# Optimization experiments

Hardware: AMD Instinct MI355X
Metric: run time of the kernel (lower is better)

The kernel has to match this reference:

```python
import jax, jax.numpy as jnp
import numpy as np

B, N, D = 4, 4096, 64   # batch, num points, point-feature channels
K = 24                  # original_k_neighbors
GO = 128                # graph_out_channel = max(32, (D*2//8)*8)
MLP = [64, 128, 256]
HALF = MLP[-1] // 2     # graph_feature_mapping out channels
EPS = 1e-5

def leaky(x):
    return jnp.where(x > 0, x, 0.2 * x)

def bn(x, gamma, beta, axes):
    # training-mode batch norm (biased variance, like torch normalization); channel last
    m = jnp.mean(x, axes, keepdims=True)
    v = jnp.var(x, axes, keepdims=True)
    return (x - m) * jax.lax.rsqrt(v + EPS) * gamma + beta

def knn_idx(p, k):
    # p: [B,N,3] -> indices of k nearest neighbors (self excluded), [B,N,k]
    sq = jnp.sum(p * p, -1)
    dist = sq[:, :, None] + sq[:, None, :] - 2.0 * jnp.einsum('bnc,bmc->bnm', p, p)
    _, idx = jax.lax.top_k(-dist, k + 1)   # smallest k+1 distances
    return idx[:, :, 1:]

def setup_inputs():
    key = jax.random.key(0)
    ks = jax.random.split(key, 8)
    w = lambda i, s: jax.random.normal(ks[i], s, jnp.float32) * 0.05
    return {
        'xyz': jax.random.normal(ks[0], (B, 3, N), jnp.float32),
        'points': jax.random.normal(ks[1], (B, D, N), jnp.float32),
        'ec_w': w(2, (GO, 2 * D)),
        'ec_g': jnp.ones((GO,), jnp.float32), 'ec_b': jnp.zeros((GO,), jnp.float32),
        'gm_w': w(3, (HALF, GO)),
        'gm_g': jnp.ones((HALF,), jnp.float32), 'gm_b': jnp.zeros((HALF,), jnp.float32),
        'w0': w(4, (MLP[0], D + 3)), 'bias0': jnp.zeros((MLP[0],), jnp.float32),
        'g0': jnp.ones((MLP[0],), jnp.float32), 'be0': jnp.zeros((MLP[0],), jnp.float32),
        'w1': w(5, (MLP[1], MLP[0])), 'bias1': jnp.zeros((MLP[1],), jnp.float32),
        'g1': jnp.ones((MLP[1],), jnp.float32), 'be1': jnp.zeros((MLP[1],), jnp.float32),
        'w2': w(6, (MLP[2], MLP[1])), 'bias2': jnp.zeros((MLP[2],), jnp.float32),
        'g2': jnp.ones((MLP[2],), jnp.float32), 'be2': jnp.zeros((MLP[2],), jnp.float32),
        'fu_w': w(7, (MLP[2], MLP[2] + HALF)),
        'fu_g': jnp.ones((MLP[2],), jnp.float32), 'fu_b': jnp.zeros((MLP[2],), jnp.float32),
    }

def reference(xyz, points, ec_w, ec_g, ec_b, gm_w, gm_g, gm_b,
              w0, bias0, g0, be0, w1, bias1, g1, be1, w2, bias2, g2, be2,
              fu_w, fu_g, fu_b):
    xyz_t = jnp.transpose(xyz, (0, 2, 1))     # [B,N,3]
    pts_t = jnp.transpose(points, (0, 2, 1))  # [B,N,D]
    edges = knn_idx(xyz_t, K)                 # [B,N,K]
    # --- EdgeConv on original graph ---
    nb = jax.vmap(lambda f, e: f[e])(pts_t, edges)  # gather: [B,N,K,D]
    ctr = pts_t[:, :, None, :]
    ef = jnp.concatenate([jnp.broadcast_to(ctr, nb.shape), nb - ctr], -1)  # [B,N,K,2D]
    h = jnp.einsum('bnkc,oc->bnko', ef, ec_w)
    h = leaky(bn(h, ec_g, ec_b, (0, 1, 2)))
    gfeat = jnp.max(h, axis=2)                # max over neighbors -> [B,N,GO]
    # --- graph_feature_mapping ---
    gm = jnp.einsum('bnc,oc->bno', gfeat, gm_w)
    gm = leaky(bn(gm, gm_g, gm_b, (0, 1)))    # [B,N,HALF]
    # --- group_all PointNet MLP ---
    g = jnp.concatenate([xyz_t, pts_t], -1)   # [B,N,D+3]
    for wl, bl, gl, bel in ((w0, bias0, g0, be0), (w1, bias1, g1, be1), (w2, bias2, g2, be2)):
        g = jax.nn.relu(bn(jnp.einsum('bnc,oc->bno', g, wl) + bl, gl, bel, (0, 1)))
    point_feat = jnp.max(g, axis=1)           # [B, MLP[-1]]
    graph_glob = jnp.max(gm, axis=1)          # [B, HALF]
    # --- fusion ---
    fused = jnp.concatenate([point_feat, graph_glob], -1)
    f = jnp.einsum('bc,oc->bo', fused, fu_w)
    f = leaky(bn(f, fu_g, fu_b, (0,)))
    return f[:, :, None]                      # [B, MLP[-1], 1]
```

## Files before the change

### kernel.cpp

```cpp
#include <hip/hip_runtime.h>

#define NPTS 4096
#define QN   16384
#define KNN  24

static constexpr size_t OFF_EDGES = 0;
static constexpr size_t OFF_BIG   = 393216;
static constexpr size_t OFF_A     = OFF_BIG;
static constexpr size_t OFF_C     = OFF_BIG + 2097152;
static constexpr size_t OFF_M     = OFF_BIG + 4194304;
static constexpr size_t OFF_GM    = OFF_BIG + 6553600;
static constexpr size_t OFF_L0    = OFF_GM + 2097152;
static constexpr size_t OFF_L1    = OFF_L0 + 1048576;
static constexpr size_t OFF_L2    = OFF_L1 + 2097152;
static constexpr size_t ST_BASE   = OFF_L2 + 4194304;
static constexpr size_t ST_BN1    = ST_BASE;
static constexpr size_t ST_GM     = ST_BASE + 256;
static constexpr size_t ST_L0     = ST_BASE + 512;
static constexpr size_t ST_L1     = ST_BASE + 640;
static constexpr size_t ST_L2     = ST_BASE + 896;
static constexpr size_t OFF_PF    = ST_BASE + 1408;
static constexpr size_t OFF_GG    = ST_BASE + 2432;
static constexpr size_t ST_TICKET = ST_BASE + 2944;
static constexpr int    ST_COUNT  = 2945;

__device__ inline unsigned fmap(float f) {
    unsigned u = __float_as_uint(f);
    return (u & 0x80000000u) ? ~u : (u | 0x80000000u);
}
__device__ inline float funmap(unsigned u) {
    unsigned v = (u & 0x80000000u) ? (u & 0x7fffffffu) : ~u;
    return __uint_as_float(v);
}

__device__ inline void xcd_decode(int v, int& b, int& t) {
    b = (v & 7) >> 1;
    t = ((v >> 3) << 1) | (v & 1);
}

template<int I, int O, int OH, int MODE, bool HASBIAS>
__device__ void layer_part(unsigned char* smem, int b, int chunk, int o0,
    const float* __restrict__ inraw, const float* __restrict__ inst, float rcnt,
    const float* __restrict__ ing, const float* __restrict__ inbe,
    const float* __restrict__ W, const float* __restrict__ bias,
    const float* __restrict__ xyz, const float* __restrict__ pts,
    float* __restrict__ outraw, float* __restrict__ outst)
{
    constexpr int OW = OH / 16;
    constexpr int OP = OH + 4;
    float* ns  = (float*)smem;
    float* nb  = ns + I;
    float* inl = nb + I;
    float* wl  = inl + 64 * 65;
    int q0 = b * 4096 + chunk * 64;

    if (MODE != 0) {
        if (threadIdx.x < I) {
            int c = threadIdx.x;
            float m = inst[c] * rcnt;
            float v = inst[I + c] * rcnt - m * m;
            float inv = 1.0f / sqrtf(v + 1e-5f);
            float sc = inv * ing[c];
            ns[c] = sc;
            nb[c] = inbe[c] - m * sc;
        }
    }

    int ng = threadIdx.x & 15, og = threadIdx.x >> 4;
    float acc[4][OW];
    #pragma unroll
    for (int r = 0; r < 4; ++r)
        #pragma unroll
        for (int i = 0; i < OW; ++i) acc[r][i] = 0.f;

    for (int ct = 0; ct < I; ct += 64) {
        int CT = (I - ct < 64) ? (I - ct) : 64;
        __syncthreads();
        if (MODE == 0) {
            for (int idx = threadIdx.x; idx < CT * 64; idx += 256) {
                int c = idx >> 6, p = idx & 63;
                int ch = ct + c;
                float v = (ch < 3) ? xyz[((size_t)(b * 3 + ch) << 12) + chunk * 64 + p]
                                   : pts[((size_t)(b * 64 + ch - 3) << 12) + chunk * 64 + p];
                inl[p * 65 + c] = v;
            }
        } else {
            const float* src = inraw + (size_t)q0 * I + ct;
            for (int idx = threadIdx.x; idx < 64 * 64; idx += 256) {
                int p = idx >> 6, c = idx & 63;
                if (c < CT) {
                    float v = fmaf(src[(size_t)p * I + c], ns[ct + c], nb[ct + c]);
                    v = (MODE == 1) ? fmaxf(v, 0.0f) : ((v > 0.0f) ? v : 0.2f * v);
                    inl[p * 65 + c] = v;
                }
            }
        }
        if (CT == 64) {
            for (int idx = threadIdx.x; idx < 64 * OH; idx += 256) {
                int o = idx >> 6, cc = idx & 63;
                wl[cc * OP + o] = W[(size_t)(o0 + o) * I + ct + cc];
            }
        } else {
            for (int idx = threadIdx.x; idx < CT * OH; idx += 256) {
                int o = idx / CT, cc = idx - o * CT;
                wl[cc * OP + o] = W[(size_t)(o0 + o) * I + ct + cc];
            }
        }
        __syncthreads();
        for (int cc = 0; cc < CT; ++cc) {
            float pv[4];
            #pragma unroll
            for (int r = 0; r < 4; ++r) pv[r] = inl[(ng * 4 + r) * 65 + cc];
            const float* wr = &wl[cc * OP + og * OW];
            if constexpr (OW == 4) {
                float4 wv = *(const float4*)wr;
                #pragma unroll
                for (int r = 0; r < 4; ++r) {
                    acc[r][0] = fmaf(pv[r], wv.x, acc[r][0]);
                    acc[r][1] = fmaf(pv[r], wv.y, acc[r][1]);
                    acc[r][2] = fmaf(pv[r], wv.z, acc[r][2]);
                    acc[r][3] = fmaf(pv[r], wv.w, acc[r][3]);
                }
            } else {
                float2 wv = *(const float2*)wr;
                #pragma unroll
                for (int r = 0; r < 4; ++r) {
                    acc[r][0] = fmaf(pv[r], wv.x, acc[r][0]);
                    acc[r][1] = fmaf(pv[r], wv.y, acc[r][1]);
                }
            }
        }
    }

    if (HASBIAS) {
        #pragma unroll
        for (int i = 0; i < OW; ++i) {
            float bv = bias[o0 + og * OW + i];
            #pragma unroll
            for (int r = 0; r < 4; ++r) acc[r][i] += bv;
        }
    }
    __syncthreads();
    #pragma unroll
    for (int r = 0; r < 4; ++r)
        #pragma unroll
        for (int i = 0; i < OW; ++i)
            wl[(ng * 4 + r) * OP + og * OW + i] = acc[r][i];
    __syncthreads();

    for (int idx = threadIdx.x; idx < 64 * OH; idx += 256) {
        int p = idx / OH, o = idx - p * OH;
        outraw[(size_t)(q0 + p) * O + o0 + o] = wl[p * OP + o];
    }
    if (threadIdx.x < OH) {
        int o = threadIdx.x;
        float s1 = 0.f, s2 = 0.f;
        #pragma unroll 8
        for (int p = 0; p < 64; ++p) {
            float v = wl[p * OP + o];
            s1 += v;
            s2 = fmaf(v, v, s2);
        }
        atomicAdd(&outst[o0 + o], s1);
        atomicAdd(&outst[O + o0 + o], s2);
    }
}

__global__ __launch_bounds__(256) void kA(const float* __restrict__ xyz,
                                          const float* __restrict__ pts,
                                          const float* __restrict__ ec_w,
                                          int* __restrict__ edges,
                                          float* __restrict__ afeat,
                                          float* __restrict__ cfeat,
                                          float* __restrict__ stz) {
    __shared__ __align__(16) unsigned char smem[25856];
    int u = blockIdx.x;
    if (u < 4096) {
        float4* cand = (float4*)smem;
        unsigned long long* bufall = (unsigned long long*)(smem + 16384);
        int b = u >> 10;
        int wave = threadIdx.x >> 6, lane = threadIdx.x & 63;
        int n = ((u & 1023) << 2) + wave;
        const float* xb = xyz + (size_t)b * 3 * 4096;
        unsigned long long* wbuf = bufall + wave * 128;

        float xq = xb[n], yq = xb[4096 + n], zq = xb[8192 + n];
        float sqq = __fadd_rn(__fadd_rn(__fmul_rn(xq, xq), __fmul_rn(yq, yq)), __fmul_rn(zq, zq));

        unsigned T = 0xFFFFFFFFu;
        int count = 0;

        auto reduce = [&]() {
            unsigned long long ka = (lane < count) ? wbuf[lane] : ~0ull;
            int ra = 0;
            if (count > 64) {
                unsigned long long kb = (lane + 64 < count) ? wbuf[lane + 64] : ~0ull;
                int rb = 0;
                for (int j = 0; j < count; ++j) {
                    unsigned long long kj = wbuf[j];
                    ra += (kj < ka);
                    rb += (kj < kb);
                }
                if (rb < 25) wbuf[rb] = kb;
            } else {
                for (int j = 0; j < count; ++j) {
                    unsigned long long kj = wbuf[j];
                    ra += (kj < ka);
                }
            }
            if (ra < 25) wbuf[ra] = ka;
            count = 25;
            T = (unsigned)(wbuf[24] >> 32);
        };

        for (int strip = 0; strip < 4; ++strip) {
            __syncthreads();
            for (int i = threadIdx.x; i < 1024; i += 256) {
                int j = strip * 1024 + i;
                float x = xb[j], y = xb[4096 + j], z = xb[8192 + j];
                float sq = __fadd_rn(__fadd_rn(__fmul_rn(x, x), __fmul_rn(y, y)), __fmul_rn(z, z));
                cand[i] = make_float4(x, y, z, sq);
            }
            __syncthreads();
            for (int t = 0; t < 16; ++t) {
                float4 cv = cand[t * 64 + lane];
                float dot = __fadd_rn(__fadd_rn(__fmul_rn(xq, cv.x), __fmul_rn(yq, cv.y)), __fmul_rn(zq, cv.z));
                float d = __fsub_rn(__fadd_rn(sqq, cv.w), __fmul_rn(2.0f, dot));
                unsigned du = fmap(d);
                bool surv = (du <= T);
                unsigned long long m = __ballot(surv);
                if (m) {
                    if (surv) {
                        int ofs = __popcll(m & ((1ull << lane) - 1ull));
                        unsigned idx = (unsigned)(strip * 1024 + t * 64 + lane);
                        wbuf[count + ofs] = ((unsigned long long)du << 32) | idx;
                    }
                    count += (int)__popcll(m);
                    if (count >= 64) reduce();
                }
            }
        }
        reduce();
        if (lane >= 1 && lane < 25)
            edges[((size_t)(b * 4096 + n)) * KNN + lane - 1] = (int)(unsigned)(wbuf[lane] & 0xFFFFFFFFull);
    } else if (u < 6144) {
        int v = u - 4096;
        int b, t;
        xcd_decode(v, b, t);
        int nchunk = t & 63, sub = t >> 6;
        int which = sub >> 2;
        int o0 = (sub & 3) * 32;
        int n0 = nchunk * 64;

        float* inl = (float*)smem;
        float* wl  = (float*)(smem + 16640);
        const float* pb = pts + (size_t)b * 64 * 4096;

        for (int idx = threadIdx.x; idx < 64 * 64; idx += 256) {
            int c = idx >> 6, p = idx & 63;
            inl[p * 65 + c] = pb[(size_t)c * 4096 + n0 + p];
        }
        for (int idx = threadIdx.x; idx < 64 * 32; idx += 256) {
            int cc = idx & 63, o = idx >> 6;
            float w2v = ec_w[(o0 + o) * 128 + 64 + cc];
            wl[cc * 36 + o] = which ? w2v : (ec_w[(o0 + o) * 128 + cc] - w2v);
        }
        __syncthreads();

        int ng = threadIdx.x & 15, og = threadIdx.x >> 4;
        float acc[4][2] = {{0.f, 0.f}, {0.f, 0.f}, {0.f, 0.f}, {0.f, 0.f}};
        for (int cc = 0; cc < 64; ++cc) {
            float pv[4];
            #pragma unroll
            for (int r = 0; r < 4; ++r) pv[r] = inl[(ng * 4 + r) * 65 + cc];
            float2 wv = *(const float2*)&wl[cc * 36 + og * 2];
            #pragma unroll
            for (int r = 0; r < 4; ++r) {
                acc[r][0] = fmaf(pv[r], wv.x, acc[r][0]);
                acc[r][1] = fmaf(pv[r], wv.y, acc[r][1]);
            }
        }
        __syncthreads();
        #pragma unroll
        for (int r = 0; r < 4; ++r) {
            wl[(ng * 4 + r) * 36 + og * 2 + 0] = acc[r][0];
            wl[(ng * 4 + r) * 36 + og * 2 + 1] = acc[r][1];
        }
        __syncthreads();
        float* dst = (which ? cfeat : afeat) + ((size_t)(b * 4096 + n0)) * 128 + o0;
        for (int idx = threadIdx.x; idx < 64 * 32; idx += 256) {
            int p = idx >> 5, o = idx & 31;
            dst[(size_t)p * 128 + o] = wl[p * 36 + o];
        }
    } else {
        for (int i = threadIdx.x; i < ST_COUNT; i += 256) stz[i] = 0.f;
    }
}

__global__ __launch_bounds__(256) void kB(const float* __restrict__ afeat,
                                          const float* __restrict__ cfeat,
                                          const int* __restrict__ edges,
                                          float* __restrict__ M,
                                          float* __restrict__ stBN1,
                                          const float* __restrict__ xyz,
                                          const float* __restrict__ pts,
                                          const float* __restrict__ w0,
                                          const float* __restrict__ bias0,
                                          float* __restrict__ l0raw,
                                          float* __restrict__ stL0) {
    __shared__ __align__(16) unsigned char smem[26368];
    int u = blockIdx.x;
    if (u < 1024) {
        int* eL = (int*)smem;
        float* red = (float*)(smem + 1536);
        int b, chunk;
        xcd_decode(u, b, chunk);
        int q0 = b * 4096 + chunk * 16;
        for (int idx = threadIdx.x; idx < 16 * KNN; idx += 256) eL[idx] = edges[(size_t)q0 * KNN + idx];
        __syncthreads();

        int m = threadIdx.x & 31;
        int g = threadIdx.x >> 5;
        int bbase = b << 12;
        float s1[4] = {0.f, 0.f, 0.f, 0.f}, s2[4] = {0.f, 0.f, 0.f, 0.f};

        #pragma unroll
        for (int half = 0; half < 2; ++half) {
            int p = g + half * 8;
            int q = q0 + p;
            float mx0 = -__builtin_inff(), mx1 = mx0, mx2 = mx0, mx3 = mx0;
            float sv0 = 0.f, sv1 = 0.f, sv2 = 0.f, sv3 = 0.f;
            float qv0 = 0.f, qv1 = 0.f, qv2 = 0.f, qv3 = 0.f;
            #pragma unroll 8
            for (int k = 0; k < KNN; ++k) {
                int e = eL[p * KNN + k];
                float4 v = *(const float4*)&cfeat[((size_t)(bbase + e) << 7) + m * 4];
                mx0 = fmaxf(mx0, v.x); sv0 += v.x; qv0 = fmaf(v.x, v.x, qv0);
                mx1 = fmaxf(mx1, v.y); sv1 += v.y; qv1 = fmaf(v.y, v.y, qv1);
                mx2 = fmaxf(mx2, v.z); sv2 += v.z; qv2 = fmaf(v.z, v.z, qv2);
                mx3 = fmaxf(mx3, v.w); sv3 += v.w; qv3 = fmaf(v.w, v.w, qv3);
            }
            float4 a = *(const float4*)&afeat[((size_t)q << 7) + m * 4];
            float4 mo = make_float4(a.x + mx0, a.y + mx1, a.z + mx2, a.w + mx3);
            *(float4*)&M[((size_t)q << 7) + m * 4] = mo;
            s1[0] += fmaf(24.f, a.x, sv0); s2[0] += 24.f * a.x * a.x + 2.f * a.x * sv0 + qv0;
            s1[1] += fmaf(24.f, a.y, sv1); s2[1] += 24.f * a.y * a.y + 2.f * a.y * sv1 + qv1;
            s1[2] += fmaf(24.f, a.z, sv2); s2[2] += 24.f * a.z * a.z + 2.f * a.z * sv2 + qv2;
            s1[3] += fmaf(24.f, a.w, sv3); s2[3] += 24.f * a.w * a.w + 2.f * a.w * sv3 + qv3;
        }
        #pragma unroll
        for (int j = 0; j < 4; ++j) red[g * 132 + m * 4 + j] = s1[j];
        __syncthreads();
        if (threadIdx.x < 128) {
            float t = 0.f;
            #pragma unroll
            for (int gg = 0; gg < 8; ++gg) t += red[gg * 132 + threadIdx.x];
            atomicAdd(&stBN1[threadIdx.x], t);
        }
        __syncthreads();
        #pragma unroll
        for (int j = 0; j < 4; ++j) red[g * 132 + m * 4 + j] = s2[j];
        __syncthreads();
        if (threadIdx.x < 128) {
            float t = 0.f;
            #pragma unroll
            for (int gg = 0; gg < 8; ++gg) t += red[gg * 132 + threadIdx.x];
            atomicAdd(&stBN1[128 + threadIdx.x], t);
        }
    } else {
        int v = u - 1024;
        int b, t;
        xcd_decode(v, b, t);
        int chunk = t & 63, y = t >> 6;
        layer_part<67, 64, 32, 0, true>(smem, b, chunk, y * 32,
            nullptr, nullptr, 0.f, nullptr, nullptr,
            w0, bias0, xyz, pts, l0raw, stL0);
    }
}

__global__ __launch_bounds__(256) void kC(const float* __restrict__ M,
                                          const float* __restrict__ stBN1,
                                          const float* __restrict__ ec_g,
                                          const float* __restrict__ ec_b,
                                          const float* __restrict__ gm_w,
                                          float* __restrict__ gmraw,
                                          float* __restrict__ stGM,
                                          const float* __restrict__ l0raw,
                                          const float* __restrict__ stL0,
                                          const float* __restrict__ g0,
                                          const float* __restrict__ be0,
                                          const float* __restrict__ w1,
                                          const float* __restrict__ bias1,
                                          float* __restrict__ l1raw,
                                          float* __restrict__ stL1) {
    __shared__ __align__(16) unsigned char smem[35072];
    int u = blockIdx.x;
    if (u < 512) {
        int b, t;
        xcd_decode(u, b, t);
        int chunk = t & 63, y = t >> 6;
        layer_part<128, 128, 64, 2, false>(smem, b, chunk, y * 64,
            M, stBN1, 1.0f / 393216.0f, ec_g, ec_b,
            gm_w, nullptr, nullptr, nullptr, gmraw, stGM);
    } else {
        int v = u - 512;
        int b, t;
        xcd_decode(v, b, t);
        int chunk = t & 63, y = t >> 6;
        layer_part<64, 128, 64, 1, true>(smem, b, chunk, y * 64,
            l0raw, stL0, 1.0f / 16384.0f, g0, be0,
            w1, bias1, nullptr, nullptr, l1raw, stL1);
    }
}

__global__ __launch_bounds__(256) void kD(const float* __restrict__ l1raw,
                                          const float* __restrict__ stL1,
                                          const float* __restrict__ g1,
                                          const float* __restrict__ be1,
                                          const float* __restrict__ w2,
                                          const float* __restrict__ bias2,
                                          float* __restrict__ l2raw,
                                          float* __restrict__ stL2) {
    __shared__ __align__(16) unsigned char smem[35072];
    int u = blockIdx.x;
    int b, t;
    xcd_decode(u, b, t);
    int chunk = t & 63, y = t >> 6;
    layer_part<128, 256, 64, 1, true>(smem, b, chunk, y * 64,
        l1raw, stL1, 1.0f / 16384.0f, g1, be1,
        w2, bias2, nullptr, nullptr, l2raw, stL2);
}

__global__ __launch_bounds__(256) void kE(const float* __restrict__ gm_raw,
                                          const float* __restrict__ stGM,
                                          const float* __restrict__ gm_g,
                                          const float* __restrict__ gm_b,
                                          const float* __restrict__ l2_raw,
                                          const float* __restrict__ stL2,
                                          const float* __restrict__ g2,
                                          const float* __restrict__ be2,
                                          unsigned* __restrict__ gg,
                                          unsigned* __restrict__ pf,
                                          unsigned* __restrict__ ticket,
                                          const float* __restrict__ fu_w,
                                          const float* __restrict__ fu_g,
                                          const float* __restrict__ fu_b,
                                          float* __restrict__ out) {
    __shared__ __align__(16) unsigned char smem[6400];
    __shared__ int isLast;
    const float rcnt = 1.0f / 16384.0f;
    int u = blockIdx.x;
    int y = u >> 5, x = u & 31;
    int b = y & 3;
    int p0 = x * 128;
    if (y < 4) {
        int o = threadIdx.x & 127, rep = threadIdx.x >> 7;
        float m = stGM[o] * rcnt;
        float v = stGM[128 + o] * rcnt - m * m;
        float sc = gm_g[o] / sqrtf(v + 1e-5f);
        float sh = gm_b[o] - m * sc;
        float mx = -__builtin_inff();
        for (int p = rep; p < 128; p += 2) {
            float xx = fmaf(gm_raw[(size_t)(b * 4096 + p0 + p) * 128 + o], sc, sh);
            xx = (xx > 0.0f) ? xx : 0.2f * xx;
            mx = fmaxf(mx, xx);
        }
        atomicMax(&gg[b * 128 + o], fmap(mx));
    } else {
        int o = threadIdx.x;
        float m = stL2[o] * rcnt;
        float v = stL2[256 + o] * rcnt - m * m;
        float sc = g2[o] / sqrtf(v + 1e-5f);
        float sh = be2[o] - m * sc;
        float mx = -__builtin_inff();
        for (int p = 0; p < 128; ++p) {
            float xx = fmaf(l2_raw[(size_t)(b * 4096 + p0 + p) * 256 + o], sc, sh);
            xx = fmaxf(xx, 0.0f);
            mx = fmaxf(mx, xx);
        }
        atomicMax(&pf[b * 256 + o], fmap(mx));
    }
    __syncthreads();
    if (threadIdx.x == 0) {
        __threadfence();
        unsigned old = atomicAdd(ticket, 1u);
        isLast = (old == 255u);
    }
    __syncthreads();
    if (isLast) {
        float* fl = (float*)smem;
        for (int idx = threadIdx.x; idx < 4 * 384; idx += 256) {
            int bb = idx / 384, c = idx - bb * 384;
            unsigned uu = (c < 256) ? atomicMax(&pf[bb * 256 + c], 0u)
                                    : atomicMax(&gg[bb * 128 + (c - 256)], 0u);
            fl[idx] = funmap(uu);
        }
        __syncthreads();
        int o = threadIdx.x;
        float f[4];
        #pragma unroll
        for (int bb = 0; bb < 4; ++bb) {
            float acc = 0.f;
            for (int c = 0; c < 384; ++c) acc = fmaf(fl[bb * 384 + c], fu_w[(size_t)o * 384 + c], acc);
            f[bb] = acc;
        }
        float m = 0.25f * (f[0] + f[1] + f[2] + f[3]);
        float var = 0.f;
        #pragma unroll
        for (int bb = 0; bb < 4; ++bb) { float tt = f[bb] - m; var = fmaf(tt, tt, var); }
        var *= 0.25f;
        float inv = 1.0f / sqrtf(var + 1e-5f);
        float gv = fu_g[o], bv = fu_b[o];
        #pragma unroll
        for (int bb = 0; bb < 4; ++bb) {
            float xx = (f[bb] - m) * inv * gv + bv;
            xx = (xx > 0.0f) ? xx : 0.2f * xx;
            out[bb * 256 + o] = xx;
        }
    }
}

extern "C" void kernel_launch(void* const* d_in, const int* in_sizes, int n_in,
                              void* d_out, int out_size, void* d_ws, size_t ws_size,
                              hipStream_t stream) {
    const float* xyz   = (const float*)d_in[0];
    const float* pts   = (const float*)d_in[1];
    const float* ec_w  = (const float*)d_in[2];
    const float* ec_g  = (const float*)d_in[3];
    const float* ec_b  = (const float*)d_in[4];
    const float* gm_w  = (const float*)d_in[5];
    const float* gm_g  = (const float*)d_in[6];
    const float* gm_b  = (const float*)d_in[7];
    const float* w0    = (const float*)d_in[8];
    const float* bias0 = (const float*)d_in[9];
    const float* g0    = (const float*)d_in[10];
    const float* be0   = (const float*)d_in[11];
    const float* w1    = (const float*)d_in[12];
    const float* bias1 = (const float*)d_in[13];
    const float* g1    = (const float*)d_in[14];
    const float* be1   = (const float*)d_in[15];
    const float* w2    = (const float*)d_in[16];
    const float* bias2 = (const float*)d_in[17];
    const float* g2    = (const float*)d_in[18];
    const float* be2   = (const float*)d_in[19];
    const float* fu_w  = (const float*)d_in[20];
    const float* fu_g  = (const float*)d_in[21];
    const float* fu_b  = (const float*)d_in[22];

    float* ws = (float*)d_ws;
    float* out = (float*)d_out;

    kA<<<6145, 256, 0, stream>>>(xyz, pts, ec_w, (int*)(ws + OFF_EDGES),
                                 ws + OFF_A, ws + OFF_C, ws + ST_BASE);
    kB<<<1536, 256, 0, stream>>>(ws + OFF_A, ws + OFF_C, (int*)(ws + OFF_EDGES),
                                 ws + OFF_M, ws + ST_BN1,
                                 xyz, pts, w0, bias0, ws + OFF_L0, ws + ST_L0);
    kC<<<1024, 256, 0, stream>>>(ws + OFF_M, ws + ST_BN1, ec_g, ec_b, gm_w,
                                 ws + OFF_GM, ws + ST_GM,
                                 ws + OFF_L0, ws + ST_L0, g0, be0, w1, bias1,
                                 ws + OFF_L1, ws + ST_L1);
    kD<<<1024, 256, 0, stream>>>(ws + OFF_L1, ws + ST_L1, g1, be1, w2, bias2,
                                 ws + OFF_L2, ws + ST_L2);
    kE<<<256, 256, 0, stream>>>(ws + OFF_GM, ws + ST_GM, gm_g, gm_b,
                                ws + OFF_L2, ws + ST_L2, g2, be2,
                                (unsigned*)(ws + OFF_GG), (unsigned*)(ws + OFF_PF),
                                (unsigned*)(ws + ST_TICKET),
                                fu_w, fu_g, fu_b, out);
}
```

Baseline: 360.4 us.

## Track per-batch raw min/max to skip materializing GM and L2 activations

The final max-pool only needs the extreme raw pre-BN values per channel and batch, because BN followed by a monotone activation is maximized at either the raw max or the raw min (depending on the sign of the scale). The GM and L2 layers now atomically record those per-batch min and max values and no longer write their full raw outputs. The final kernel collapses to a single block that reads the extremes. Separately, the layer tiles are widened to cover all output channels per block, with transposed smem layouts and float4 loads. This removes large global writes and rereads, at the cost of more atomics, larger shared memory per block and fewer blocks.

Measured after the change: 320.4 us. -11.1%, faster.

```diff
diff --git a/kernel.cpp b/kernel.cpp
--- a/kernel.cpp
+++ b/kernel.cpp
@@ -9,20 +9,19 @@
 static constexpr size_t OFF_A     = OFF_BIG;
 static constexpr size_t OFF_C     = OFF_BIG + 2097152;
 static constexpr size_t OFF_M     = OFF_BIG + 4194304;
-static constexpr size_t OFF_GM    = OFF_BIG + 6553600;
-static constexpr size_t OFF_L0    = OFF_GM + 2097152;
+static constexpr size_t OFF_L0    = OFF_BIG + 6553600;
 static constexpr size_t OFF_L1    = OFF_L0 + 1048576;
-static constexpr size_t OFF_L2    = OFF_L1 + 2097152;
-static constexpr size_t ST_BASE   = OFF_L2 + 4194304;
+static constexpr size_t ST_BASE   = OFF_L1 + 2097152;
 static constexpr size_t ST_BN1    = ST_BASE;
 static constexpr size_t ST_GM     = ST_BASE + 256;
 static constexpr size_t ST_L0     = ST_BASE + 512;
 static constexpr size_t ST_L1     = ST_BASE + 640;
 static constexpr size_t ST_L2     = ST_BASE + 896;
-static constexpr size_t OFF_PF    = ST_BASE + 1408;
-static constexpr size_t OFF_GG    = ST_BASE + 2432;
-static constexpr size_t ST_TICKET = ST_BASE + 2944;
-static constexpr int    ST_COUNT  = 2945;
+static constexpr size_t RMX_GM    = ST_BASE + 1408;
+static constexpr size_t RMN_GM    = ST_BASE + 1920;
+static constexpr size_t RMX_L2    = ST_BASE + 2432;
+static constexpr size_t RMN_L2    = ST_BASE + 3456;
+static constexpr int    ST_COUNT  = 4480;
 
 __device__ inline unsigned fmap(float f) {
     unsigned u = __float_as_uint(f);
@@ -38,20 +37,21 @@
     t = ((v >> 3) << 1) | (v & 1);
 }
 
-template<int I, int O, int OH, int MODE, bool HASBIAS>
+template<int I, int O, int OH, int MODE, bool HASBIAS, bool WRITE_RAW, bool MINMAX>
 __device__ void layer_part(unsigned char* smem, int b, int chunk, int o0,
     const float* __restrict__ inraw, const float* __restrict__ inst, float rcnt,
     const float* __restrict__ ing, const float* __restrict__ inbe,
     const float* __restrict__ W, const float* __restrict__ bias,
     const float* __restrict__ xyz, const float* __restrict__ pts,
-    float* __restrict__ outraw, float* __restrict__ outst)
+    float* __restrict__ outraw, float* __restrict__ outst,
+    unsigned* __restrict__ rmax, unsigned* __restrict__ rmin)
 {
+    constexpr int OP = OH + 4;
     constexpr int OW = OH / 16;
-    constexpr int OP = OH + 4;
     float* ns  = (float*)smem;
     float* nb  = ns + I;
-    float* inl = nb + I;
-    float* wl  = inl + 64 * 65;
+    float* inl = (float*)(smem + 1024);
+    float* wl  = (float*)(smem + 1024 + 17408);
     int q0 = b * 4096 + chunk * 64;
 
     if (MODE != 0) {
@@ -82,23 +82,40 @@
                 int ch = ct + c;
                 float v = (ch < 3) ? xyz[((size_t)(b * 3 + ch) << 12) + chunk * 64 + p]
                                    : pts[((size_t)(b * 64 + ch - 3) << 12) + chunk * 64 + p];
-                inl[p * 65 + c] = v;
+                inl[c * 68 + p] = v;
             }
         } else {
             const float* src = inraw + (size_t)q0 * I + ct;
-            for (int idx = threadIdx.x; idx < 64 * 64; idx += 256) {
-                int p = idx >> 6, c = idx & 63;
-                if (c < CT) {
-                    float v = fmaf(src[(size_t)p * I + c], ns[ct + c], nb[ct + c]);
-                    v = (MODE == 1) ? fmaxf(v, 0.0f) : ((v > 0.0f) ? v : 0.2f * v);
-                    inl[p * 65 + c] = v;
+            #pragma unroll
+            for (int it = 0; it < 4; ++it) {
+                int idx = threadIdx.x + it * 256;
+                int c = idx & 63, pq = idx >> 6;
+                float sc_ = ns[ct + c], sh_ = nb[ct + c];
+                float4 v;
+                v.x = fmaf(src[(size_t)(pq * 4 + 0) * I + c], sc_, sh_);
+                v.y = fmaf(src[(size_t)(pq * 4 + 1) * I + c], sc_, sh_);
+                v.z = fmaf(src[(size_t)(pq * 4 + 2) * I + c], sc_, sh_);
+                v.w = fmaf(src[(size_t)(pq * 4 + 3) * I + c], sc_, sh_);
+                if (MODE == 1) {
+                    v.x = fmaxf(v.x, 0.f); v.y = fmaxf(v.y, 0.f);
+                    v.z = fmaxf(v.z, 0.f); v.w = fmaxf(v.w, 0.f);
+                } else {
+                    v.x = (v.x > 0.f) ? v.x : 0.2f * v.x;
+                    v.y = (v.y > 0.f) ? v.y : 0.2f * v.y;
+                    v.z = (v.z > 0.f) ? v.z : 0.2f * v.z;
+                    v.w = (v.w > 0.f) ? v.w : 0.2f * v.w;
                 }
-            }
-        }
-        if (CT == 64) {
-            for (int idx = threadIdx.x; idx < 64 * OH; idx += 256) {
-                int o = idx >> 6, cc = idx & 63;
-                wl[cc * OP + o] = W[(size_t)(o0 + o) * I + ct + cc];
+                *(float4*)&inl[c * 68 + pq * 4] = v;
+            }
+        }
+        if ((I & 3) == 0) {
+            for (int idx = threadIdx.x; idx < (CT / 4) * OH; idx += 256) {
+                int cq = idx & 15, o = idx >> 4;
+                float4 wv4 = *(const float4*)&W[(size_t)(o0 + o) * I + ct + cq * 4];
+                wl[(cq * 4 + 0) * OP + o] = wv4.x;
+                wl[(cq * 4 + 1) * OP + o] = wv4.y;
+                wl[(cq * 4 + 2) * OP + o] = wv4.z;
+                wl[(cq * 4 + 3) * OP + o] = wv4.w;
             }
         } else {
             for (int idx = threadIdx.x; idx < CT * OH; idx += 256) {
@@ -108,25 +125,17 @@
         }
         __syncthreads();
         for (int cc = 0; cc < CT; ++cc) {
-            float pv[4];
-            #pragma unroll
-            for (int r = 0; r < 4; ++r) pv[r] = inl[(ng * 4 + r) * 65 + cc];
-            const float* wr = &wl[cc * OP + og * OW];
-            if constexpr (OW == 4) {
-                float4 wv = *(const float4*)wr;
+            float4 pv = *(const float4*)&inl[cc * 68 + ng * 4];
+            float pvv[4] = {pv.x, pv.y, pv.z, pv.w};
+            #pragma unroll
+            for (int i4 = 0; i4 < OW / 4; ++i4) {
+                float4 wv = *(const float4*)&wl[cc * OP + og * OW + i4 * 4];
                 #pragma unroll
                 for (int r = 0; r < 4; ++r) {
-                    acc[r][0] = fmaf(pv[r], wv.x, acc[r][0]);
-                    acc[r][1] = fmaf(pv[r], wv.y, acc[r][1]);
-                    acc[r][2] = fmaf(pv[r], wv.z, acc[r][2]);
-                    acc[r][3] = fmaf(pv[r], wv.w, acc[r][3]);
-                }
-            } else {
-                float2 wv = *(const float2*)wr;
-                #pragma unroll
-                for (int r = 0; r < 4; ++r) {
-                    acc[r][0] = fmaf(pv[r], wv.x, acc[r][0]);
-                    acc[r][1] = fmaf(pv[r], wv.y, acc[r][1]);
+                    acc[r][i4 * 4 + 0] = fmaf(pvv[r], wv.x, acc[r][i4 * 4 + 0]);
+                    acc[r][i4 * 4 + 1] = fmaf(pvv[r], wv.y, acc[r][i4 * 4 + 1]);
+                    acc[r][i4 * 4 + 2] = fmaf(pvv[r], wv.z, acc[r][i4 * 4 + 2]);
+                    acc[r][i4 * 4 + 3] = fmaf(pvv[r], wv.w, acc[r][i4 * 4 + 3]);
                 }
             }
         }
@@ -148,21 +157,29 @@
             wl[(ng * 4 + r) * OP + og * OW + i] = acc[r][i];
     __syncthreads();
 
-    for (int idx = threadIdx.x; idx < 64 * OH; idx += 256) {
-        int p = idx / OH, o = idx - p * OH;
-        outraw[(size_t)(q0 + p) * O + o0 + o] = wl[p * OP + o];
+    if (WRITE_RAW) {
+        for (int idx = threadIdx.x; idx < 64 * OH; idx += 256) {
+            int p = idx / OH, o = idx - p * OH;
+            outraw[(size_t)(q0 + p) * O + o0 + o] = wl[p * OP + o];
+        }
     }
     if (threadIdx.x < OH) {
         int o = threadIdx.x;
         float s1 = 0.f, s2 = 0.f;
+        float mx = -__builtin_inff(), mn = __builtin_inff();
         #pragma unroll 8
         for (int p = 0; p < 64; ++p) {
             float v = wl[p * OP + o];
             s1 += v;
             s2 = fmaf(v, v, s2);
+            if (MINMAX) { mx = fmaxf(mx, v); mn = fminf(mn, v); }
         }
         atomicAdd(&outst[o0 + o], s1);
         atomicAdd(&outst[O + o0 + o], s2);
+        if (MINMAX) {
+            atomicMax(&rmax[b * O + o0 + o], fmap(mx));
+            atomicMin(&rmin[b * O + o0 + o], fmap(mn));
+        }
     }
 }
 
@@ -172,7 +189,7 @@
                                           int* __restrict__ edges,
                                           float* __restrict__ afeat,
                                           float* __restrict__ cfeat,
-                                          float* __restrict__ stz) {
+                                          unsigned* __restrict__ stz) {
     __shared__ __align__(16) unsigned char smem[25856];
     int u = blockIdx.x;
     if (u < 4096) {
@@ -293,7 +310,11 @@
             dst[(size_t)p * 128 + o] = wl[p * 36 + o];
         }
     } else {
-        for (int i = threadIdx.x; i < ST_COUNT; i += 256) stz[i] = 0.f;
+        for (int i = threadIdx.x; i < ST_COUNT; i += 256) {
+            bool sentinel = (i >= (int)(RMN_GM - ST_BASE) && i < (int)(RMX_L2 - ST_BASE)) ||
+                            (i >= (int)(RMN_L2 - ST_BASE));
+            stz[i] = sentinel ? 0xFFFFFFFFu : 0u;
+        }
     }
 }
 
@@ -308,7 +329,7 @@
                                           const float* __restrict__ bias0,
                                           float* __restrict__ l0raw,
                                           float* __restrict__ stL0) {
-    __shared__ __align__(16) unsigned char smem[26368];
+    __shared__ __align__(16) unsigned char smem[35840];
     int u = blockIdx.x;
     if (u < 1024) {
         int* eL = (int*)smem;
@@ -369,12 +390,11 @@
         }
     } else {
         int v = u - 1024;
-        int b, t;
-        xcd_decode(v, b, t);
-        int chunk = t & 63, y = t >> 6;
-        layer_part<67, 64, 32, 0, true>(smem, b, chunk, y * 32,
+        int b, chunk;
+        xcd_decode(v, b, chunk);
+        layer_part<67, 64, 64, 0, true, true, false>(smem, b, chunk, 0,
             nullptr, nullptr, 0.f, nullptr, nullptr,
-            w0, bias0, xyz, pts, l0raw, stL0);
+            w0, bias0, xyz, pts, l0raw, stL0, nullptr, nullptr);
     }
 }
 
@@ -383,8 +403,9 @@
                                           const float* __restrict__ ec_g,
                                           const float* __restrict__ ec_b,
                                           const float* __restrict__ gm_w,
-                                          float* __restrict__ gmraw,
                                           float* __restrict__ stGM,
+                                          unsigned* __restrict__ rmxGM,
+                                          unsigned* __restrict__ rmnGM,
                                           const float* __restrict__ l0raw,
                                           const float* __restrict__ stL0,
                                           const float* __restrict__ g0,
@@ -393,23 +414,21 @@
                                           const float* __restrict__ bias1,
                                           float* __restrict__ l1raw,
                                           float* __restrict__ stL1) {
-    __shared__ __align__(16) unsigned char smem[35072];
+    __shared__ __align__(16) unsigned char smem[52224];
     int u = blockIdx.x;
-    if (u < 512) {
-        int b, t;
-        xcd_decode(u, b, t);
-        int chunk = t & 63, y = t >> 6;
-        layer_part<128, 128, 64, 2, false>(smem, b, chunk, y * 64,
+    if (u < 256) {
+        int b, chunk;
+        xcd_decode(u, b, chunk);
+        layer_part<128, 128, 128, 2, false, false, true>(smem, b, chunk, 0,
             M, stBN1, 1.0f / 393216.0f, ec_g, ec_b,
-            gm_w, nullptr, nullptr, nullptr, gmraw, stGM);
+            gm_w, nullptr, nullptr, nullptr, nullptr, stGM, rmxGM, rmnGM);
     } else {
-        int v = u - 512;
-        int b, t;
-        xcd_decode(v, b, t);
-        int chunk = t & 63, y = t >> 6;
-        layer_part<64, 128, 64, 1, true>(smem, b, chunk, y * 64,
+        int v = u - 256;
+        int b, chunk;
+        xcd_decode(v, b, chunk);
+        layer_part<64, 128, 128, 1, true, true, false>(smem, b, chunk, 0,
             l0raw, stL0, 1.0f / 16384.0f, g0, be0,
-            w1, bias1, nullptr, nullptr, l1raw, stL1);
+            w1, bias1, nullptr, nullptr, l1raw, stL1, nullptr, nullptr);
     }
 }
 
@@ -419,104 +438,85 @@
                                           const float* __restrict__ be1,
                                           const float* __restrict__ w2,
                                           const float* __restrict__ bias2,
-                                          float* __restrict__ l2raw,
-                                          float* __restrict__ stL2) {
-    __shared__ __align__(16) unsigned char smem[35072];
+                                          float* __restrict__ stL2,
+                                          unsigned* __restrict__ rmxL2,
+                                          unsigned* __restrict__ rmnL2) {
+    __shared__ __align__(16) unsigned char smem[52224];
     int u = blockIdx.x;
     int b, t;
     xcd_decode(u, b, t);
     int chunk = t & 63, y = t >> 6;
-    layer_part<128, 256, 64, 1, true>(smem, b, chunk, y * 64,
+    layer_part<128, 256, 128, 1, true, false, true>(smem, b, chunk, y * 128,
         l1raw, stL1, 1.0f / 16384.0f, g1, be1,
-        w2, bias2, nullptr, nullptr, l2raw, stL2);
-}
-
-__global__ __launch_bounds__(256) void kE(const float* __restrict__ gm_raw,
-                                          const float* __restrict__ stGM,
+        w2, bias2, nullptr, nullptr, nullptr, stL2, rmxL2, rmnL2);
+}
+
+__global__ __launch_bounds__(256) void kE(const float* __restrict__ stGM,
                                           const float* __restrict__ gm_g,
                                           const float* __restrict__ gm_b,
-                                          const float* __restrict__ l2_raw,
+                                          const unsigned* __restrict__ rmxGM,
+                                          const unsigned* __restrict__ rmnGM,
                                           const float* __restrict__ stL2,
                                           const float* __restrict__ g2,
                                           const float* __restrict__ be2,
-                                          unsigned* __restrict__ gg,
-                                          unsigned* __restrict__ pf,
-                                          unsigned* __restrict__ ticket,
+                                          const unsigned* __restrict__ rmxL2,
+                                          const unsigned* __restrict__ rmnL2,
                                           const float* __restrict__ fu_w,
                                           const float* __restrict__ fu_g,
                                           const float* __restrict__ fu_b,
                                           float* __restrict__ out) {
-    __shared__ __align__(16) unsigned char smem[6400];
-    __shared__ int isLast;
-    const float rcnt = 1.0f / 16384.0f;
-    int u = blockIdx.x;
-    int y = u >> 5, x = u & 31;
-    int b = y & 3;
-    int p0 = x * 128;
-    if (y < 4) {
-        int o = threadIdx.x & 127, rep = threadIdx.x >> 7;
-        float m = stGM[o] * rcnt;
-        float v = stGM[128 + o] * rcnt - m * m;
+    __shared__ float fl[4 * 384];
+    const float rc = 1.0f / 16384.0f;
+    int t = threadIdx.x;
+    {
+        int o = t;
+        float m = stL2[o] * rc;
+        float v = stL2[256 + o] * rc - m * m;
+        float sc = g2[o] / sqrtf(v + 1e-5f);
+        float sh = be2[o] - m * sc;
+        #pragma unroll
+        for (int b = 0; b < 4; ++b) {
+            float f1 = fmaxf(fmaf(funmap(rmxL2[b * 256 + o]), sc, sh), 0.f);
+            float f2 = fmaxf(fmaf(funmap(rmnL2[b * 256 + o]), sc, sh), 0.f);
+            fl[b * 384 + o] = fmaxf(f1, f2);
+        }
+    }
+    if (t < 128) {
+        int o = t;
+        float m = stGM[o] * rc;
+        float v = stGM[128 + o] * rc - m * m;
         float sc = gm_g[o] / sqrtf(v + 1e-5f);
         float sh = gm_b[o] - m * sc;
-        float mx = -__builtin_inff();
-        for (int p = rep; p < 128; p += 2) {
-            float xx = fmaf(gm_raw[(size_t)(b * 4096 + p0 + p) * 128 + o], sc, sh);
-            xx = (xx > 0.0f) ? xx : 0.2f * xx;
-            mx = fmaxf(mx, xx);
-        }
-        atomicMax(&gg[b * 128 + o], fmap(mx));
-    } else {
-        int o = threadIdx.x;
-        float m = stL2[o] * rcnt;
-        float v = stL2[256 + o] * rcnt - m * m;
-        float sc = g2[o] / sqrtf(v + 1e-5f);
-        float sh = be2[o] - m * sc;
-        float mx = -__builtin_inff();
-        for (int p = 0; p < 128; ++p) {
-            float xx = fmaf(l2_raw[(size_t)(b * 4096 + p0 + p) * 256 + o], sc, sh);
-            xx = fmaxf(xx, 0.0f);
-            mx = fmaxf(mx, xx);
-        }
-        atomicMax(&pf[b * 256 + o], fmap(mx));
+        #pragma unroll
+        for (int b = 0; b < 4; ++b) {
+            float x1 = fmaf(funmap(rmxGM[b * 128 + o]), sc, sh);
+            x1 = (x1 > 0.f) ? x1 : 0.2f * x1;
+            float x2 = fmaf(funmap(rmnGM[b * 128 + o]), sc, sh);
+            x2 = (x2 > 0.f) ? x2 : 0.2f * x2;
+            fl[b * 384 + 256 + o] = fmaxf(x1, x2);
+        }
     }
     __syncthreads();
-    if (threadIdx.x == 0) {
-        __threadfence();
-        unsigned old = atomicAdd(ticket, 1u);
-        isLast = (old == 255u);
-    }
-    __syncthreads();
-    if (isLast) {
-        float* fl = (float*)smem;
-        for (int idx = threadIdx.x; idx < 4 * 384; idx += 256) {
-            int bb = idx / 384, c = idx - bb * 384;
-            unsigned uu = (c < 256) ? atomicMax(&pf[bb * 256 + c], 0u)
-                                    : atomicMax(&gg[bb * 128 + (c - 256)], 0u);
-            fl[idx] = funmap(uu);
-        }
-        __syncthreads();
-        int o = threadIdx.x;
-        float f[4];
-        #pragma unroll
-        for (int bb = 0; bb < 4; ++bb) {
-            float acc = 0.f;
-            for (int c = 0; c < 384; ++c) acc = fmaf(fl[bb * 384 + c], fu_w[(size_t)o * 384 + c], acc);
-            f[bb] = acc;
-        }
-        float m = 0.25f * (f[0] + f[1] + f[2] + f[3]);
-        float var = 0.f;
-        #pragma unroll
-        for (int bb = 0; bb < 4; ++bb) { float tt = f[bb] - m; var = fmaf(tt, tt, var); }
-        var *= 0.25f;
-        float inv = 1.0f / sqrtf(var + 1e-5f);
-        float gv = fu_g[o], bv = fu_b[o];
-        #pragma unroll
-        for (int bb = 0; bb < 4; ++bb) {
-            float xx = (f[bb] - m) * inv * gv + bv;
-            xx = (xx > 0.0f) ? xx : 0.2f * xx;
-            out[bb * 256 + o] = xx;
-        }
+    int o = t;
+    float f[4];
+    #pragma unroll
+    for (int bb = 0; bb < 4; ++bb) {
+        float acc = 0.f;
+        for (int c = 0; c < 384; ++c) acc = fmaf(fl[bb * 384 + c], fu_w[(size_t)o * 384 + c], acc);
+        f[bb] = acc;
+    }
+    float m = 0.25f * (f[0] + f[1] + f[2] + f[3]);
+    float var = 0.f;
+    #pragma unroll
+    for (int bb = 0; bb < 4; ++bb) { float tt = f[bb] - m; var = fmaf(tt, tt, var); }
+    var *= 0.25f;
+    float inv = 1.0f / sqrtf(var + 1e-5f);
+    float gv = fu_g[o], bv = fu_b[o];
+    #pragma unroll
+    for (int bb = 0; bb < 4; ++bb) {
+        float xx = (f[bb] - m) * inv * gv + bv;
+        xx = (xx > 0.0f) ? xx : 0.2f * xx;
+        out[bb * 256 + o] = xx;
     }
 }
 
@@ -551,19 +551,19 @@
     float* out = (float*)d_out;
 
     kA<<<6145, 256, 0, stream>>>(xyz, pts, ec_w, (int*)(ws + OFF_EDGES),
-                                 ws + OFF_A, ws + OFF_C, ws + ST_BASE);
-    kB<<<1536, 256, 0, stream>>>(ws + OFF_A, ws + OFF_C, (int*)(ws + OFF_EDGES),
+                                 ws + OFF_A, ws + OFF_C, (unsigned*)(ws + ST_BASE));
+    kB<<<1280, 256, 0, stream>>>(ws + OFF_A, ws + OFF_C, (int*)(ws + OFF_EDGES),
                                  ws + OFF_M, ws + ST_BN1,
                                  xyz, pts, w0, bias0, ws + OFF_L0, ws + ST_L0);
-    kC<<<1024, 256, 0, stream>>>(ws + OFF_M, ws + ST_BN1, ec_g, ec_b, gm_w,
-                                 ws + OFF_GM, ws + ST_GM,
-                                 ws + OFF_L0, ws + ST_L0, g0, be0, w1, bias1,
-                                 ws + OFF_L1, ws + ST_L1);
-    kD<<<1024, 256, 0, stream>>>(ws + OFF_L1, ws + ST_L1, g1, be1, w2, bias2,
-                                 ws + OFF_L2, ws + ST_L2);
-    kE<<<256, 256, 0, stream>>>(ws + OFF_GM, ws + ST_GM, gm_g, gm_b,
-                                ws + OFF_L2, ws + ST_L2, g2, be2,
-                                (unsigned*)(ws + OFF_GG), (unsigned*)(ws + OFF_PF),
-                                (unsigned*)(ws + ST_TICKET),
-                                fu_w, fu_g, fu_b, out);
-}
+    kC<<<512, 256, 0, stream>>>(ws + OFF_M, ws + ST_BN1, ec_g, ec_b, gm_w,
+                                ws + ST_GM, (unsigned*)(ws + RMX_GM), (unsigned*)(ws + RMN_GM),
+                                ws + OFF_L0, ws + ST_L0, g0, be0, w1, bias1,
+                                ws + OFF_L1, ws + ST_L1);
+    kD<<<512, 256, 0, stream>>>(ws + OFF_L1, ws + ST_L1, g1, be1, w2, bias2,
+                                ws + ST_L2, (unsigned*)(ws + RMX_L2), (unsigned*)(ws + RMN_L2));
+    kE<<<1, 256, 0, stream>>>(ws + ST_GM, gm_g, gm_b,
+                              (unsigned*)(ws + RMX_GM), (unsigned*)(ws + RMN_GM),
+                              ws + ST_L2, g2, be2,
+                              (unsigned*)(ws + RMX_L2), (unsigned*)(ws + RMN_L2),
+                              fu_w, fu_g, fu_b, out);
+}
```
